# Optimization experiments

Measured on AMD Instinct MI355X. Metric: run time of the kernel, lower is better.

Reference implementation:

```python
import jax, jax.numpy as jnp
import numpy as np

NL = 256
NP = 8192
NV = 16
B = 2


def _xavier(key, shape):
    fan_in, fan_out = shape[-2], shape[-1]
    lim = np.sqrt(6.0 / (fan_in + fan_out))
    return jax.random.uniform(key, shape, jnp.float32, -lim, lim)


def setup_inputs() -> dict:
    key = jax.random.key(0)
    ks = jax.random.split(key, 12)
    return {
        "nodes": jax.random.normal(ks[0], (B, NP, NL), jnp.float32),
        "edges_attributes": jax.random.normal(ks[1], (NP, NV, NL), jnp.float32),
        "edges_indices": jax.random.randint(ks[2], (NP, NV), 0, NP, jnp.int64) if jax.config.jax_enable_x64 else jax.random.randint(ks[2], (NP, NV), 0, NP).astype(jnp.int32),
        # edge MLP (dim_in=3*NL, nb_hidden=3 -> first + 2 hidden + last)
        "e_fw": _xavier(ks[3], (3 * NL, NL)), "e_fb": jnp.zeros((NL,), jnp.float32),
        "e_hw": _xavier(ks[4], (2, NL, NL)), "e_hb": jnp.zeros((2, NL), jnp.float32),
        "e_lw": _xavier(ks[5], (NL, NL)), "e_lb": jnp.zeros((NL,), jnp.float32),
        # node MLP (dim_in=2*NL)
        "n_fw": _xavier(ks[6], (2 * NL, NL)), "n_fb": jnp.zeros((NL,), jnp.float32),
        "n_hw": _xavier(ks[7], (2, NL, NL)), "n_hb": jnp.zeros((2, NL), jnp.float32),
        "n_lw": _xavier(ks[8], (NL, NL)), "n_lb": jnp.zeros((NL,), jnp.float32),
    }


def _mlp(x, fw, fb, hw, hb, lw, lb):
    x = jax.nn.relu(x @ fw + fb)
    for i in range(hw.shape[0]):  # fixed small number of hidden layers
        x = jax.nn.relu(x @ hw[i] + hb[i])
    return x @ lw + lb


def reference(nodes, edges_attributes, edges_indices,
              e_fw, e_fb, e_hw, e_hb, e_lw, e_lb,
              n_fw, n_fb, n_hw, n_hb, n_lw, n_lb):
    b, npts, nl = nodes.shape
    nv = edges_indices.shape[1]
    # gather neighbor features: [B, Np, Nv, Nl]
    nodes_nb = jnp.take(nodes, edges_indices, axis=1)
    # self features broadcast over neighbor axis, edge attrs broadcast over batch
    self_exp = jnp.broadcast_to(nodes[:, :, None, :], (b, npts, nv, nl))
    edge_exp = jnp.broadcast_to(edges_attributes[None], (b, npts, nv, nl))
    concat_msg = jnp.concatenate([self_exp, nodes_nb, edge_exp], axis=-1)  # [B,Np,Nv,3Nl]
    new_edges = _mlp(concat_msg, e_fw, e_fb, e_hw, e_hb, e_lw, e_lb)  # [B,Np,Nv,Nl]
    agg = jnp.sum(new_edges, axis=2)  # [B,Np,Nl]
    concat_nodes = jnp.concatenate([nodes, agg], axis=-1)  # [B,Np,2Nl]
    new_nodes = nodes + _mlp(concat_nodes, n_fw, n_fb, n_hw, n_hb, n_lw, n_lb)
    return new_nodes, new_edges[0]
```

## Files before the change

kernel.cpp:

```cpp
#include <hip/hip_runtime.h>
#include <hip/hip_bf16.h>


typedef __bf16 bf16;
typedef __bf16 bf16x8 __attribute__((ext_vector_type(8)));
typedef float f32x4 __attribute__((ext_vector_type(4)));

#define MFMA16(a, b, c) __builtin_amdgcn_mfma_f32_16x16x32_bf16((a), (b), (c), 0, 0, 0)

constexpr int kNP = 8192;
constexpr int kNV = 16;

__global__ __launch_bounds__(256) void pack_all(
    const float* __restrict__ e_fw, const float* __restrict__ e_hw,
    const float* __restrict__ e_lw, const float* __restrict__ n_fw,
    const float* __restrict__ n_hw, const float* __restrict__ n_lw,
    bf16* __restrict__ wp) {
  int t = blockIdx.x * 256 + threadIdx.x;
  const float* src;
  int kd = 8, local;
  if (t < 196608) {
    src = e_fw + (t >> 16) * 65536; local = t & 65535;
  } else if (t < 262144) { src = e_hw;           local = t - 196608;
  } else if (t < 327680) { src = e_hw + 65536;   local = t - 262144;
  } else if (t < 393216) { src = e_lw;           local = t - 327680;
  } else if (t < 524288) { src = n_fw;           local = t - 393216; kd = 16;
  } else if (t < 589824) { src = n_hw;           local = t - 524288;
  } else if (t < 655360) { src = n_hw + 65536;   local = t - 589824;
  } else               { src = n_lw;             local = t - 655360; }
  int j = local & 7;
  int l = (local >> 3) & 63;
  int r2 = local >> 9;
  int ks = r2 % kd;
  int nt = r2 / kd;
  int k = ks * 32 + ((l >> 4) << 3) + j;
  int n = (nt << 4) + (l & 15);
  wp[t] = (bf16)src[k * 256 + n];
}

template <int KD, int MT>
__device__ __forceinline__ void layer_acc(const bf16* X, int xs,
                                          const bf16* __restrict__ Wp,
                                          const float* __restrict__ bias,
                                          f32x4 (&acc)[MT][4], int rowOff,
                                          int wc) {
  const int lane = threadIdx.x & 63;
  const int q = lane >> 4;
  const int c = lane & 15;
#pragma unroll
  for (int nt = 0; nt < 4; nt++) {
    float bv = bias ? bias[wc * 64 + nt * 16 + c] : 0.0f;
#pragma unroll
    for (int mt = 0; mt < MT; mt++) {
      acc[mt][nt][0] = bv; acc[mt][nt][1] = bv;
      acc[mt][nt][2] = bv; acc[mt][nt][3] = bv;
    }
  }
#pragma unroll
  for (int ks = 0; ks < KD; ks++) {
    bf16x8 a[MT];
#pragma unroll
    for (int mt = 0; mt < MT; mt++)
      a[mt] = *(const bf16x8*)(X + (rowOff + mt * 16 + c) * xs + ks * 32 + q * 8);
    bf16x8 bb[4];
#pragma unroll
    for (int nt = 0; nt < 4; nt++)
      bb[nt] = *(const bf16x8*)(Wp + ((((wc * 4 + nt) * KD + ks) * 64 + lane) << 3));
#pragma unroll
    for (int mt = 0; mt < MT; mt++)
#pragma unroll
      for (int nt = 0; nt < 4; nt++)
        acc[mt][nt] = MFMA16(a[mt], bb[nt], acc[mt][nt]);
  }
}

template <int KD, int MT, bool RELU>
__device__ __forceinline__ void layer_inplace(bf16* X, int xs_r, int xs_w,
                                              const bf16* __restrict__ Wp,
                                              const float* __restrict__ bias,
                                              int rowOff, int wc) {
  f32x4 acc[MT][4];
  layer_acc<KD, MT>(X, xs_r, Wp, bias, acc, rowOff, wc);
  const int lane = threadIdx.x & 63;
  const int q = lane >> 4;
  const int c = lane & 15;
  __syncthreads();
#pragma unroll
  for (int mt = 0; mt < MT; mt++)
#pragma unroll
    for (int nt = 0; nt < 4; nt++)
#pragma unroll
      for (int i = 0; i < 4; i++) {
        float v = acc[mt][nt][i];
        if (RELU) v = fmaxf(v, 0.0f);
        X[(rowOff + mt * 16 + q * 4 + i) * xs_w + (wc * 64 + nt * 16 + c)] = (bf16)v;
      }
  __syncthreads();
}

__global__ __launch_bounds__(512, 4) void producer_gemm(
    const float* __restrict__ nodes, const float* __restrict__ eattr,
    const bf16* __restrict__ w_self, const bf16* __restrict__ w_nb,
    const bf16* __restrict__ w_ea, const float* __restrict__ e_fb,
    bf16* __restrict__ Sb, bf16* __restrict__ Pb, bf16* __restrict__ Eb) {
  __shared__ bf16 X[64 * 280];
  const int t = threadIdx.x;
  const int m0 = blockIdx.x * 64;
  const float* A; const float* bias = nullptr; const bf16* Wp; bf16* out;
  if (m0 < 16384)      { A = nodes + m0 * 256;           Wp = w_self; bias = e_fb; out = Sb + m0 * 256; }
  else if (m0 < 32768) { A = nodes + (m0 - 16384) * 256; Wp = w_nb;   out = Pb + (m0 - 16384) * 256; }
  else                 { A = eattr + (m0 - 32768) * 256; Wp = w_ea;   out = Eb + (m0 - 32768) * 256; }
  const int r = t >> 3;
  const int q8 = t & 7;
#pragma unroll
  for (int c8 = 0; c8 < 4; c8++) {
    int col = q8 * 8 + c8 * 64;
    float4 f0 = *(const float4*)(A + r * 256 + col);
    float4 f1 = *(const float4*)(A + r * 256 + col + 4);
    bf16x8 v;
    v[0] = (bf16)f0.x; v[1] = (bf16)f0.y; v[2] = (bf16)f0.z; v[3] = (bf16)f0.w;
    v[4] = (bf16)f1.x; v[5] = (bf16)f1.y; v[6] = (bf16)f1.z; v[7] = (bf16)f1.w;
    *(bf16x8*)(X + r * 280 + col) = v;
  }
  __syncthreads();
  const int w = t >> 6;
  layer_inplace<8, 2, false>(X, 280, 280, Wp, bias, (w >> 2) * 32, w & 3);
#pragma unroll
  for (int c8 = 0; c8 < 4; c8++) {
    int col = q8 * 8 + c8 * 64;
    *(uint4*)(out + r * 256 + col) = *(const uint4*)(X + r * 280 + col);
  }
}

__global__ __launch_bounds__(512, 4) void edge_mlp(
    const bf16* __restrict__ S, const bf16* __restrict__ P,
    const bf16* __restrict__ E, const int* __restrict__ idx,
    const bf16* __restrict__ Wh0, const bf16* __restrict__ Wh1,
    const bf16* __restrict__ Wl, const float* __restrict__ e_hb,
    const float* __restrict__ e_lb, bf16* __restrict__ agg,
    float* __restrict__ out_edges) {
  __shared__ bf16 X[64 * 280];
  const int t = threadIdx.x;
  const int e0 = blockIdx.x * 64;
  const int b = e0 >> 17;
  const int pbase = (e0 >> 4) & (kNP - 1);
  {
    const int r = t >> 3;
    const int q8 = t & 7;
    const int p = pbase + (r >> 4);
    const int v = r & 15;
    const int nb = idx[p * kNV + v];
    const bf16* Srow = S + ((b << 13) + p) * 256;
    const bf16* Prow = P + ((b << 13) + nb) * 256;
    const bf16* Erow = E + (p * kNV + v) * 256;
#pragma unroll
    for (int c8 = 0; c8 < 4; c8++) {
      int col = q8 * 8 + c8 * 64;
      bf16x8 sv = *(const bf16x8*)(Srow + col);
      bf16x8 pv = *(const bf16x8*)(Prow + col);
      bf16x8 ev = *(const bf16x8*)(Erow + col);
      bf16x8 o;
#pragma unroll
      for (int j = 0; j < 8; j++) {
        float f = (float)sv[j] + (float)pv[j] + (float)ev[j];
        o[j] = (bf16)fmaxf(f, 0.0f);
      }
      *(bf16x8*)(X + r * 280 + col) = o;
    }
  }
  __syncthreads();
  const int w = t >> 6;
  const int wc = w & 3;
  const int rowOff = (w >> 2) * 32;
  layer_inplace<8, 2, true>(X, 280, 280, Wh0, e_hb, rowOff, wc);
  layer_inplace<8, 2, true>(X, 280, 280, Wh1, e_hb + 256, rowOff, wc);
  f32x4 acc[2][4];
  layer_acc<8, 2>(X, 280, Wl, e_lb, acc, rowOff, wc);
  const int lane = t & 63;
  const int q = lane >> 4;
  const int c = lane & 15;
#pragma unroll
  for (int mt = 0; mt < 2; mt++) {
#pragma unroll
    for (int nt = 0; nt < 4; nt++) {
      float s = acc[mt][nt][0] + acc[mt][nt][1] + acc[mt][nt][2] + acc[mt][nt][3];
      s += __shfl_xor(s, 16, 64);
      s += __shfl_xor(s, 32, 64);
      if (lane < 16)
        agg[((b << 13) + pbase + (rowOff >> 4) + mt) * 256 + wc * 64 + nt * 16 + lane] = (bf16)s;
    }
  }
  if (b == 0) {
#pragma unroll
    for (int mt = 0; mt < 2; mt++)
#pragma unroll
      for (int nt = 0; nt < 4; nt++)
#pragma unroll
        for (int i = 0; i < 4; i++) {
          int e = e0 + rowOff + mt * 16 + q * 4 + i;
          out_edges[e * 256 + (wc * 64 + nt * 16 + c)] = acc[mt][nt][i];
        }
  }
}

__global__ __launch_bounds__(512, 4) void node_mlp(
    const float* __restrict__ nodes, const bf16* __restrict__ agg,
    const bf16* __restrict__ Wf, const bf16* __restrict__ Wh0,
    const bf16* __restrict__ Wh1, const bf16* __restrict__ Wl,
    const float* __restrict__ n_fb, const float* __restrict__ n_hb,
    const float* __restrict__ n_lb, float* __restrict__ out_nodes) {
  __shared__ bf16 X[32 * 536];
  const int t = threadIdx.x;
  const int r = t >> 4;
  const int q16 = t & 15;
  const int m = blockIdx.x * 32 + r;
#pragma unroll
  for (int c8 = 0; c8 < 4; c8++) {
    int col = q16 * 8 + c8 * 128;
    if (col < 256) {
      float4 f0 = *(const float4*)(nodes + m * 256 + col);
      float4 f1 = *(const float4*)(nodes + m * 256 + col + 4);
      bf16x8 v;
      v[0] = (bf16)f0.x; v[1] = (bf16)f0.y; v[2] = (bf16)f0.z; v[3] = (bf16)f0.w;
      v[4] = (bf16)f1.x; v[5] = (bf16)f1.y; v[6] = (bf16)f1.z; v[7] = (bf16)f1.w;
      *(bf16x8*)(X + r * 536 + col) = v;
    } else {
      *(bf16x8*)(X + r * 536 + col) =
          *(const bf16x8*)(agg + m * 256 + (col - 256));
    }
  }
  __syncthreads();
  const int w = t >> 6;
  const int wc = w & 3;
  const int rowOff = (w >> 2) * 16;
  layer_inplace<16, 1, true>(X, 536, 280, Wf, n_fb, rowOff, wc);
  layer_inplace<8, 1, true>(X, 280, 280, Wh0, n_hb, rowOff, wc);
  layer_inplace<8, 1, true>(X, 280, 280, Wh1, n_hb + 256, rowOff, wc);
  f32x4 acc[1][4];
  layer_acc<8, 1>(X, 280, Wl, n_lb, acc, rowOff, wc);
  const int lane = t & 63;
  const int q = lane >> 4;
  const int c = lane & 15;
#pragma unroll
  for (int nt = 0; nt < 4; nt++)
#pragma unroll
    for (int i = 0; i < 4; i++) {
      int mm = blockIdx.x * 32 + rowOff + q * 4 + i;
      int col = wc * 64 + nt * 16 + c;
      out_nodes[mm * 256 + col] = nodes[mm * 256 + col] + acc[0][nt][i];
    }
}

extern "C" void kernel_launch(void* const* d_in, const int* in_sizes, int n_in,
                              void* d_out, int out_size, void* d_ws,
                              size_t ws_size, hipStream_t stream) {
  const float* nodes = (const float*)d_in[0];
  const float* eattr = (const float*)d_in[1];
  const int* eidx = (const int*)d_in[2];
  const float* e_fw = (const float*)d_in[3];
  const float* e_fb = (const float*)d_in[4];
  const float* e_hw = (const float*)d_in[5];
  const float* e_hb = (const float*)d_in[6];
  const float* e_lw = (const float*)d_in[7];
  const float* e_lb = (const float*)d_in[8];
  const float* n_fw = (const float*)d_in[9];
  const float* n_fb = (const float*)d_in[10];
  const float* n_hw = (const float*)d_in[11];
  const float* n_hb = (const float*)d_in[12];
  const float* n_lw = (const float*)d_in[13];
  const float* n_lb = (const float*)d_in[14];

  char* ws = (char*)d_ws;
  bf16* Sb = (bf16*)(ws + 0);
  bf16* Pb = (bf16*)(ws + 8388608);
  bf16* Eb = (bf16*)(ws + 16777216);
  bf16* aggb = (bf16*)(ws + 83886080);
  bf16* wp = (bf16*)(ws + 92274688);
  bf16* w_self = wp;
  bf16* w_nb = wp + 65536;
  bf16* w_ea = wp + 131072;
  bf16* w_eh0 = wp + 196608;
  bf16* w_eh1 = wp + 262144;
  bf16* w_el = wp + 327680;
  bf16* w_nf = wp + 393216;
  bf16* w_nh0 = wp + 524288;
  bf16* w_nh1 = wp + 589824;
  bf16* w_nl = wp + 655360;

  float* out_nodes = (float*)d_out;
  float* out_edges = (float*)d_out + 4194304;

  pack_all<<<2816, 256, 0, stream>>>(e_fw, e_hw, e_lw, n_fw, n_hw, n_lw, wp);
  producer_gemm<<<2560, 512, 0, stream>>>(nodes, eattr, w_self, w_nb, w_ea,
                                          e_fb, Sb, Pb, Eb);
  edge_mlp<<<4096, 512, 0, stream>>>(Sb, Pb, Eb, eidx, w_eh0, w_eh1, w_el,
                                     e_hb, e_lb, aggb, out_edges);
  node_mlp<<<512, 512, 0, stream>>>(nodes, aggb, w_nf, w_nh0, w_nh1, w_nl,
                                    n_fb, n_hb, n_lb, out_nodes);
}
```

Measured before the change: 480.9 us.

## Fuse edge-attribute projection into edge MLP and share node reads for S/P

The edge-attribute GEMM (eattr @ W_ea) moves into the edge MLP kernel. Each block now handles two points across both batches, so the 32 edge rows are projected once and reused for both batch elements instead of being written to and re-read from a global Eb buffer. The producer kernel now computes both the self and neighbor projections from a single staged node tile, which halves the node loads. The cost is an extra small GEMM plus additional barriers inside the edge kernel, and less parallelism in the producer.

```diff
diff --git a/kernel.cpp b/kernel.cpp
--- a/kernel.cpp
+++ b/kernel.cpp
@@ -98,107 +98,158 @@
   __syncthreads();
 }
 
-__global__ __launch_bounds__(512, 4) void producer_gemm(
-    const float* __restrict__ nodes, const float* __restrict__ eattr,
-    const bf16* __restrict__ w_self, const bf16* __restrict__ w_nb,
-    const bf16* __restrict__ w_ea, const float* __restrict__ e_fb,
-    bf16* __restrict__ Sb, bf16* __restrict__ Pb, bf16* __restrict__ Eb) {
+__global__ __launch_bounds__(512, 4) void producer_sp(
+    const float* __restrict__ nodes, const bf16* __restrict__ w_self,
+    const bf16* __restrict__ w_nb, const float* __restrict__ e_fb,
+    bf16* __restrict__ Sb, bf16* __restrict__ Pb) {
   __shared__ bf16 X[64 * 280];
   const int t = threadIdx.x;
   const int m0 = blockIdx.x * 64;
-  const float* A; const float* bias = nullptr; const bf16* Wp; bf16* out;
-  if (m0 < 16384)      { A = nodes + m0 * 256;           Wp = w_self; bias = e_fb; out = Sb + m0 * 256; }
-  else if (m0 < 32768) { A = nodes + (m0 - 16384) * 256; Wp = w_nb;   out = Pb + (m0 - 16384) * 256; }
-  else                 { A = eattr + (m0 - 32768) * 256; Wp = w_ea;   out = Eb + (m0 - 32768) * 256; }
-  const int r = t >> 3;
-  const int q8 = t & 7;
-#pragma unroll
-  for (int c8 = 0; c8 < 4; c8++) {
-    int col = q8 * 8 + c8 * 64;
-    float4 f0 = *(const float4*)(A + r * 256 + col);
-    float4 f1 = *(const float4*)(A + r * 256 + col + 4);
-    bf16x8 v;
-    v[0] = (bf16)f0.x; v[1] = (bf16)f0.y; v[2] = (bf16)f0.z; v[3] = (bf16)f0.w;
-    v[4] = (bf16)f1.x; v[5] = (bf16)f1.y; v[6] = (bf16)f1.z; v[7] = (bf16)f1.w;
-    *(bf16x8*)(X + r * 280 + col) = v;
-  }
-  __syncthreads();
-  const int w = t >> 6;
-  layer_inplace<8, 2, false>(X, 280, 280, Wp, bias, (w >> 2) * 32, w & 3);
-#pragma unroll
-  for (int c8 = 0; c8 < 4; c8++) {
-    int col = q8 * 8 + c8 * 64;
-    *(uint4*)(out + r * 256 + col) = *(const uint4*)(X + r * 280 + col);
-  }
-}
-
-__global__ __launch_bounds__(512, 4) void edge_mlp(
-    const bf16* __restrict__ S, const bf16* __restrict__ P,
-    const bf16* __restrict__ E, const int* __restrict__ idx,
-    const bf16* __restrict__ Wh0, const bf16* __restrict__ Wh1,
-    const bf16* __restrict__ Wl, const float* __restrict__ e_hb,
-    const float* __restrict__ e_lb, bf16* __restrict__ agg,
-    float* __restrict__ out_edges) {
-  __shared__ bf16 X[64 * 280];
-  const int t = threadIdx.x;
-  const int e0 = blockIdx.x * 64;
-  const int b = e0 >> 17;
-  const int pbase = (e0 >> 4) & (kNP - 1);
   {
     const int r = t >> 3;
     const int q8 = t & 7;
-    const int p = pbase + (r >> 4);
-    const int v = r & 15;
+#pragma unroll
+    for (int c8 = 0; c8 < 4; c8++) {
+      int col = q8 * 8 + c8 * 64;
+      float4 f0 = *(const float4*)(nodes + (m0 + r) * 256 + col);
+      float4 f1 = *(const float4*)(nodes + (m0 + r) * 256 + col + 4);
+      bf16x8 v;
+      v[0] = (bf16)f0.x; v[1] = (bf16)f0.y; v[2] = (bf16)f0.z; v[3] = (bf16)f0.w;
+      v[4] = (bf16)f1.x; v[5] = (bf16)f1.y; v[6] = (bf16)f1.z; v[7] = (bf16)f1.w;
+      *(bf16x8*)(X + r * 280 + col) = v;
+    }
+  }
+  __syncthreads();
+  const int lane = t & 63;
+  const int w = t >> 6;
+  const int wc = w & 3;
+  const int rowOff = (w >> 2) * 32;
+  const int q = lane >> 4;
+  const int c = lane & 15;
+  f32x4 acc[2][4];
+  layer_acc<8, 2>(X, 280, w_self, e_fb, acc, rowOff, wc);
+#pragma unroll
+  for (int mt = 0; mt < 2; mt++)
+#pragma unroll
+    for (int nt = 0; nt < 4; nt++)
+#pragma unroll
+      for (int i = 0; i < 4; i++)
+        Sb[(m0 + rowOff + mt * 16 + q * 4 + i) * 256 + wc * 64 + nt * 16 + c] =
+            (bf16)acc[mt][nt][i];
+  layer_acc<8, 2>(X, 280, w_nb, nullptr, acc, rowOff, wc);
+#pragma unroll
+  for (int mt = 0; mt < 2; mt++)
+#pragma unroll
+    for (int nt = 0; nt < 4; nt++)
+#pragma unroll
+      for (int i = 0; i < 4; i++)
+        Pb[(m0 + rowOff + mt * 16 + q * 4 + i) * 256 + wc * 64 + nt * 16 + c] =
+            (bf16)acc[mt][nt][i];
+}
+
+__global__ __launch_bounds__(512, 4) void edge_mlp(
+    const bf16* __restrict__ S, const bf16* __restrict__ P,
+    const float* __restrict__ eattr, const int* __restrict__ idx,
+    const bf16* __restrict__ w_ea, const bf16* __restrict__ Wh0,
+    const bf16* __restrict__ Wh1, const bf16* __restrict__ Wl,
+    const float* __restrict__ e_hb, const float* __restrict__ e_lb,
+    bf16* __restrict__ agg, float* __restrict__ out_edges) {
+  __shared__ bf16 X[64 * 280];
+  const int t = threadIdx.x;
+  const int pbase = blockIdx.x * 2;
+  {
+    const int r = t >> 4;
+    const int q16 = t & 15;
+    const float* src = eattr + (pbase * 16 + r) * 256 + q16 * 16;
+    bf16* dst = X + (32 + r) * 280 + q16 * 16;
+    float4 f0 = *(const float4*)(src);
+    float4 f1 = *(const float4*)(src + 4);
+    float4 f2 = *(const float4*)(src + 8);
+    float4 f3 = *(const float4*)(src + 12);
+    bf16x8 v0, v1;
+    v0[0] = (bf16)f0.x; v0[1] = (bf16)f0.y; v0[2] = (bf16)f0.z; v0[3] = (bf16)f0.w;
+    v0[4] = (bf16)f1.x; v0[5] = (bf16)f1.y; v0[6] = (bf16)f1.z; v0[7] = (bf16)f1.w;
+    v1[0] = (bf16)f2.x; v1[1] = (bf16)f2.y; v1[2] = (bf16)f2.z; v1[3] = (bf16)f2.w;
+    v1[4] = (bf16)f3.x; v1[5] = (bf16)f3.y; v1[6] = (bf16)f3.z; v1[7] = (bf16)f3.w;
+    *(bf16x8*)(dst) = v0;
+    *(bf16x8*)(dst + 8) = v1;
+  }
+  __syncthreads();
+  const int lane = t & 63;
+  const int w = t >> 6;
+  const int wc = w & 3;
+  const int rg = w >> 2;
+  const int q = lane >> 4;
+  const int c = lane & 15;
+  {
+    f32x4 acce[1][4];
+    layer_acc<8, 1>(X, 280, w_ea, nullptr, acce, 32 + rg * 16, wc);
+    __syncthreads();
+#pragma unroll
+    for (int nt = 0; nt < 4; nt++)
+#pragma unroll
+      for (int i = 0; i < 4; i++)
+        X[(32 + rg * 16 + q * 4 + i) * 280 + wc * 64 + nt * 16 + c] =
+            (bf16)acce[0][nt][i];
+  }
+  __syncthreads();
+  {
+    const int r = t >> 3;
+    const int q8 = t & 7;
+    const int b = r >> 5;
+    const int rr = r & 31;
+    const int p = pbase + (rr >> 4);
+    const int v = rr & 15;
     const int nb = idx[p * kNV + v];
     const bf16* Srow = S + ((b << 13) + p) * 256;
     const bf16* Prow = P + ((b << 13) + nb) * 256;
-    const bf16* Erow = E + (p * kNV + v) * 256;
-#pragma unroll
-    for (int c8 = 0; c8 < 4; c8++) {
-      int col = q8 * 8 + c8 * 64;
+    bf16x8 hold[4];
+#pragma unroll
+    for (int j = 0; j < 4; j++) {
+      int col = q8 * 32 + j * 8;
+      bf16x8 ev = *(const bf16x8*)(X + (32 + rr) * 280 + col);
       bf16x8 sv = *(const bf16x8*)(Srow + col);
       bf16x8 pv = *(const bf16x8*)(Prow + col);
-      bf16x8 ev = *(const bf16x8*)(Erow + col);
       bf16x8 o;
 #pragma unroll
-      for (int j = 0; j < 8; j++) {
-        float f = (float)sv[j] + (float)pv[j] + (float)ev[j];
-        o[j] = (bf16)fmaxf(f, 0.0f);
+      for (int k = 0; k < 8; k++) {
+        float f = (float)sv[k] + (float)pv[k] + (float)ev[k];
+        o[k] = (bf16)fmaxf(f, 0.0f);
       }
-      *(bf16x8*)(X + r * 280 + col) = o;
-    }
-  }
-  __syncthreads();
-  const int w = t >> 6;
-  const int wc = w & 3;
-  const int rowOff = (w >> 2) * 32;
-  layer_inplace<8, 2, true>(X, 280, 280, Wh0, e_hb, rowOff, wc);
-  layer_inplace<8, 2, true>(X, 280, 280, Wh1, e_hb + 256, rowOff, wc);
+      hold[j] = o;
+    }
+    __syncthreads();
+#pragma unroll
+    for (int j = 0; j < 4; j++)
+      *(bf16x8*)(X + r * 280 + q8 * 32 + j * 8) = hold[j];
+  }
+  __syncthreads();
+  layer_inplace<8, 2, true>(X, 280, 280, Wh0, e_hb, rg * 32, wc);
+  layer_inplace<8, 2, true>(X, 280, 280, Wh1, e_hb + 256, rg * 32, wc);
   f32x4 acc[2][4];
-  layer_acc<8, 2>(X, 280, Wl, e_lb, acc, rowOff, wc);
-  const int lane = t & 63;
-  const int q = lane >> 4;
-  const int c = lane & 15;
+  layer_acc<8, 2>(X, 280, Wl, e_lb, acc, rg * 32, wc);
 #pragma unroll
   for (int mt = 0; mt < 2; mt++) {
+    const int g = rg * 2 + mt;
 #pragma unroll
     for (int nt = 0; nt < 4; nt++) {
       float s = acc[mt][nt][0] + acc[mt][nt][1] + acc[mt][nt][2] + acc[mt][nt][3];
       s += __shfl_xor(s, 16, 64);
       s += __shfl_xor(s, 32, 64);
       if (lane < 16)
-        agg[((b << 13) + pbase + (rowOff >> 4) + mt) * 256 + wc * 64 + nt * 16 + lane] = (bf16)s;
-    }
-  }
-  if (b == 0) {
+        agg[(((g >> 1) << 13) + pbase + (g & 1)) * 256 + wc * 64 + nt * 16 + lane] =
+            (bf16)s;
+    }
+  }
+  if (rg == 0) {
 #pragma unroll
     for (int mt = 0; mt < 2; mt++)
 #pragma unroll
       for (int nt = 0; nt < 4; nt++)
 #pragma unroll
         for (int i = 0; i < 4; i++) {
-          int e = e0 + rowOff + mt * 16 + q * 4 + i;
-          out_edges[e * 256 + (wc * 64 + nt * 16 + c)] = acc[mt][nt][i];
+          int e = (pbase + mt) * kNV + q * 4 + i;
+          out_edges[e * 256 + wc * 64 + nt * 16 + c] = acc[mt][nt][i];
         }
   }
 }
@@ -273,9 +324,8 @@
   char* ws = (char*)d_ws;
   bf16* Sb = (bf16*)(ws + 0);
   bf16* Pb = (bf16*)(ws + 8388608);
-  bf16* Eb = (bf16*)(ws + 16777216);
-  bf16* aggb = (bf16*)(ws + 83886080);
-  bf16* wp = (bf16*)(ws + 92274688);
+  bf16* aggb = (bf16*)(ws + 16777216);
+  bf16* wp = (bf16*)(ws + 25165824);
   bf16* w_self = wp;
   bf16* w_nb = wp + 65536;
   bf16* w_ea = wp + 131072;
@@ -291,10 +341,9 @@
   float* out_edges = (float*)d_out + 4194304;
 
   pack_all<<<2816, 256, 0, stream>>>(e_fw, e_hw, e_lw, n_fw, n_hw, n_lw, wp);
-  producer_gemm<<<2560, 512, 0, stream>>>(nodes, eattr, w_self, w_nb, w_ea,
-                                          e_fb, Sb, Pb, Eb);
-  edge_mlp<<<4096, 512, 0, stream>>>(Sb, Pb, Eb, eidx, w_eh0, w_eh1, w_el,
-                                     e_hb, e_lb, aggb, out_edges);
+  producer_sp<<<256, 512, 0, stream>>>(nodes, w_self, w_nb, e_fb, Sb, Pb);
+  edge_mlp<<<4096, 512, 0, stream>>>(Sb, Pb, eattr, eidx, w_ea, w_eh0, w_eh1,
+                                     w_el, e_hb, e_lb, aggb, out_edges);
   node_mlp<<<512, 512, 0, stream>>>(nodes, aggb, w_nf, w_nh0, w_nh1, w_nl,
                                     n_fb, n_hb, n_lb, out_nodes);
 }
```

Measured after the change: 471.9 us. About the same (-1.9%).
